# Kernel tuning notes

Measured on AMD Instinct MI355X. Metric: run time of the kernel, lower is better.

Reference implementation:

```python
import jax, jax.numpy as jnp
import numpy as np

B, F, D = 1024, 256, 64  # batch, featureNumb, featureDim


def setup_inputs() -> dict:
    key = jax.random.key(0)
    k1, k2, k3, k4 = jax.random.split(key, 4)
    feature = jax.random.normal(k1, (B, F, D), dtype=jnp.float32)
    indicator = jax.random.normal(k2, (F, D), dtype=jnp.float32)
    # QKVTransformV2(n, D, D): n stacked DxD linear maps of the indicator
    W_qk = jax.random.normal(k3, (2, D, D), dtype=jnp.float32) / np.float32(np.sqrt(D))
    W_qkv = jax.random.normal(k4, (3, D, D), dtype=jnp.float32) / np.float32(np.sqrt(D))
    return {"feature": feature, "indicator": indicator, "W_qk": W_qk, "W_qkv": W_qkv}


def reference(feature, indicator, W_qk, W_qkv):
    d = indicator.shape[-1]
    scale = jnp.asarray(1.0 / np.sqrt(d), feature.dtype)

    # --- gate branch: QKTrans + DotWeight + LTE (straight-through hard threshold) ---
    trans = jnp.einsum('fd,nde->nfe', indicator, W_qk)            # [2,F,D]
    gate_logits = jnp.einsum('id,jd->ij', trans[0], trans[1]) * scale  # [F,F]
    gate = (gate_logits > 0).astype(feature.dtype)                # LTE forward: hard 0/1 gate

    # --- QKV branch, fused form of the rank-1 outer products ---
    # Original: QKV_outer[t,i,j] = qkv[t,i] (x) qkv[t,j]  (DxD rank-1)
    #           input[b,t,i,j,:] = feature[b,i] @ QKV_outer[t,i,j]
    #                            = (feature[b,i] . qkv[t,i]) * qkv[t,j]
    qkv = jnp.einsum('fd,nde->nfe', indicator, W_qkv)             # [3,F,D]
    s = jnp.einsum('bfd,nfd->nbf', feature, qkv)                  # s[t,b,i] = feature[b,i].qkv[t,i]

    # score[b,i,j] = input[b,0,i,j,:] . input[b,1,j,i,:]
    #              = s[0,b,i] * s[1,b,j] * (qkv[1,i] . qkv[0,j])
    cross = jnp.einsum('id,jd->ij', qkv[1], qkv[0])               # [F,F]
    score = s[0][:, :, None] * s[1][:, None, :] * cross[None]     # [B,F,F]
    scoreHat = score * gate[None]                                 # [B,F,F]

    # output[b,i,:] = sum_j scoreHat[b,i,j] * value[b,i,j,:]
    #               = s[2,b,i] * sum_j scoreHat[b,i,j] * qkv[2,j,:]
    out = s[2][:, :, None] * jnp.einsum('bij,jd->bid', scoreHat, qkv[2])  # [B,F,D]
    return out
```

## Files before the change

### kernel.cpp

```cpp
#include <hip/hip_runtime.h>
#include <stdint.h>

#define B 1024
#define F 256
#define D 64

typedef __attribute__((ext_vector_type(8))) short short8;
typedef __attribute__((ext_vector_type(4))) float f32x4;

__device__ __forceinline__ short f2bf(float f) {
    unsigned u = __builtin_bit_cast(unsigned, f);
    u += 0x7fff + ((u >> 16) & 1);
    return (short)(u >> 16);
}
__device__ __forceinline__ float bf2f(short s) {
    unsigned u = ((unsigned)(unsigned short)s) << 16;
    return __builtin_bit_cast(float, u);
}
__device__ __forceinline__ unsigned pk_bf16(float a, float b) {
    unsigned ua = __builtin_bit_cast(unsigned, a) + 0x8000u;
    unsigned ub = __builtin_bit_cast(unsigned, b) + 0x8000u;
    return __builtin_amdgcn_perm(ub, ua, 0x07060302u);
}

__device__ __forceinline__ float dot4(float4 a, float4 b) {
    return a.x * b.x + a.y * b.y + a.z * b.z + a.w * b.w;
}


__global__ void precompute_trans(const float* __restrict__ indicator,
                                 const float* __restrict__ W_qk,
                                 const float* __restrict__ W_qkv,
                                 float* __restrict__ trans,
                                 float* __restrict__ qkv) {
    int idx = blockIdx.x * blockDim.x + threadIdx.x;
    int n   = idx / (F * D);
    int rem = idx - n * (F * D);
    int f   = rem / D;
    int e   = rem - f * D;
    const float* W = (n < 2) ? (W_qk + n * D * D) : (W_qkv + (n - 2) * D * D);
    const float* ind = indicator + f * D;
    float acc = 0.f;
#pragma unroll 8
    for (int d = 0; d < D; ++d) acc += ind[d] * W[d * D + e];
    if (n < 2) trans[n * F * D + f * D + e] = acc;
    else       qkv[(n - 2) * F * D + f * D + e] = acc;
}

__global__ __launch_bounds__(256) void compute_Mt(const float* __restrict__ trans,
                                                  const float* __restrict__ qkv,
                                                  short* __restrict__ At,
                                                  short* __restrict__ q2K) {
    int j = blockIdx.x;
    int i = threadIdx.x;
    const float4* t0 = (const float4*)(trans + i * D);
    const float4* t1 = (const float4*)(trans + F * D + j * D);
    const float4* q1 = (const float4*)(qkv + F * D + i * D);
    const float4* q0 = (const float4*)(qkv + j * D);
    float d0 = 0.f, d1 = 0.f;
#pragma unroll
    for (int k = 0; k < D / 4; ++k) {
        float4 a = t0[k], b = t1[k], c = q1[k], e = q0[k];
        d0 += dot4(a, b);
        d1 += dot4(c, e);
    }
    float v = (d0 > 0.f) ? d1 : 0.f;
    At[((j >> 5) * F + i) * 32 + (j & 31)] = f2bf(v);
    if (j < D) {
        int p = (j & 3) * 16 + (j >> 2);
        q2K[((i >> 5) * D + p) * 32 + (i & 31)] = f2bf(qkv[2 * F * D + i * D + j]);
    }
}

__global__ __launch_bounds__(512, 4) void fused_sg(const float* __restrict__ feature,
                                                   const float* __restrict__ qkv,
                                                   const short* __restrict__ At,
                                                   const short* __restrict__ q2K,
                                                   float* __restrict__ out) {
    int bp  = blockIdx.x;
    int b0  = bp * 2;
    int tid = threadIdx.x;

    __shared__ __align__(16) short q2L[8 * 64 * 32];
    __shared__ __align__(16) short s1L[2 * F];
    __shared__ __align__(16) float gL[2 * F];

    {
        const float4* Qg = (const float4*)q2K;
        float4* Ql = (float4*)q2L;
#pragma unroll
        for (int v = tid; v < 2048; v += 512) Ql[v] = Qg[v];
    }

    {
        int rg = tid >> 4;
        int l  = tid & 15;
#pragma unroll 2
        for (int p = 0; p < 8; ++p) {
            int f = p * 32 + rg;
            float4 fv0 = ((const float4*)(feature + ((size_t)(b0 * F + f)) * D))[l];
            float4 fv1 = ((const float4*)(feature + ((size_t)((b0 + 1) * F + f)) * D))[l];
            float4 q0 = ((const float4*)(qkv + f * D))[l];
            float4 q1 = ((const float4*)(qkv + F * D + f * D))[l];
            float4 q2 = ((const float4*)(qkv + 2 * F * D + f * D))[l];
            float a00 = dot4(fv0, q0);
            float a01 = dot4(fv0, q1);
            float a02 = dot4(fv0, q2);
            float a10 = dot4(fv1, q0);
            float a11 = dot4(fv1, q1);
            float a12 = dot4(fv1, q2);
#pragma unroll
            for (int m = 1; m < 16; m <<= 1) {
                a00 += __shfl_xor(a00, m, 64);
                a01 += __shfl_xor(a01, m, 64);
                a02 += __shfl_xor(a02, m, 64);
                a10 += __shfl_xor(a10, m, 64);
                a11 += __shfl_xor(a11, m, 64);
                a12 += __shfl_xor(a12, m, 64);
            }
            if (l == 0) {
                gL[f]      = a00 * a02;
                gL[F + f]  = a10 * a12;
                s1L[f]     = f2bf(a01);
                s1L[F + f] = f2bf(a11);
            }
        }
    }
    __syncthreads();

    int w    = tid >> 6;
    int lane = tid & 63;
    int l16  = lane & 15;
    int lq   = lane >> 4;
    int kq   = lq * 8;
    int wc   = w & 1;
    int it   = w >> 1;
    int b    = b0 + wc;

    f32x4 acc[4][4];
#pragma unroll
    for (int mt = 0; mt < 4; ++mt)
#pragma unroll
        for (int nt = 0; nt < 4; ++nt) acc[mt][nt] = (f32x4){0.f, 0.f, 0.f, 0.f};

    for (int jt = 0; jt < F / 32; ++jt) {
        short8 sv = *(const short8*)(s1L + wc * F + jt * 32 + kq);
        float sf[8];
#pragma unroll
        for (int e = 0; e < 8; ++e) sf[e] = bf2f(sv[e]);

        short8 bfr[4];
#pragma unroll
        for (int nt = 0; nt < 4; ++nt) {
            int d = nt * 16 + l16;
            short8 qv = *(const short8*)(q2L + (jt * 64 + d) * 32 + kq);
            int4 packed;
            packed.x = pk_bf16(bf2f(qv[0]) * sf[0], bf2f(qv[1]) * sf[1]);
            packed.y = pk_bf16(bf2f(qv[2]) * sf[2], bf2f(qv[3]) * sf[3]);
            packed.z = pk_bf16(bf2f(qv[4]) * sf[4], bf2f(qv[5]) * sf[5]);
            packed.w = pk_bf16(bf2f(qv[6]) * sf[6], bf2f(qv[7]) * sf[7]);
            bfr[nt] = __builtin_bit_cast(short8, packed);
        }
#pragma unroll
        for (int mt = 0; mt < 4; ++mt) {
            short8 af = *(const short8*)(At + ((size_t)jt * F + it * 64 + mt * 16 + l16) * 32 + kq);
#pragma unroll
            for (int nt = 0; nt < 4; ++nt)
                acc[mt][nt] = __builtin_amdgcn_mfma_f32_16x16x32_bf16(
                    af, bfr[nt], acc[mt][nt], 0, 0, 0);
        }
    }

    const float4* g4 = (const float4*)(gL + wc * F + it * 64);
#pragma unroll
    for (int mt = 0; mt < 4; ++mt) {
        float4 gg = g4[mt * 4 + lq];
        float* obase = out + ((size_t)(b * F + it * 64 + mt * 16 + lq * 4)) * D + l16 * 4;
        float4 v0 = {gg.x * acc[mt][0][0], gg.x * acc[mt][1][0],
                     gg.x * acc[mt][2][0], gg.x * acc[mt][3][0]};
        float4 v1 = {gg.y * acc[mt][0][1], gg.y * acc[mt][1][1],
                     gg.y * acc[mt][2][1], gg.y * acc[mt][3][1]};
        float4 v2 = {gg.z * acc[mt][0][2], gg.z * acc[mt][1][2],
                     gg.z * acc[mt][2][2], gg.z * acc[mt][3][2]};
        float4 v3 = {gg.w * acc[mt][0][3], gg.w * acc[mt][1][3],
                     gg.w * acc[mt][2][3], gg.w * acc[mt][3][3]};
        *(float4*)(obase + 0 * D) = v0;
        *(float4*)(obase + 1 * D) = v1;
        *(float4*)(obase + 2 * D) = v2;
        *(float4*)(obase + 3 * D) = v3;
    }
}

extern "C" void kernel_launch(void* const* d_in, const int* in_sizes, int n_in,
                              void* d_out, int out_size, void* d_ws, size_t ws_size,
                              hipStream_t stream) {
    const float* feature   = (const float*)d_in[0];
    const float* indicator = (const float*)d_in[1];
    const float* W_qk      = (const float*)d_in[2];
    const float* W_qkv     = (const float*)d_in[3];
    float* out = (float*)d_out;

    float* ws    = (float*)d_ws;
    float* trans = ws;
    float* qkv   = trans + 2 * F * D;
    short* At    = (short*)(qkv + 3 * F * D);
    short* q2K   = At + F * F;

    hipLaunchKernelGGL(precompute_trans, dim3((5 * F * D) / 256), dim3(256), 0,
                       stream, indicator, W_qk, W_qkv, trans, qkv);
    hipLaunchKernelGGL(compute_Mt, dim3(F), dim3(256), 0, stream, trans, qkv, At, q2K);
    hipLaunchKernelGGL(fused_sg, dim3(B / 2), dim3(512), 0, stream,
                       feature, qkv, At, q2K, out);
}
```

Measured before the change: 144.9 us.

## Double-buffer feature rows into LDS via async global_load_lds in fused_sg

The feature-projection phase now streams each batch pair's feature rows into a double-buffered LDS staging area with direct global-to-LDS loads, in 64-row chunks. This overlaps the next chunk's load with the current chunk's dot products. It adds 32KB of shared memory per block and lowers the launch-bounds occupancy hint from 4 to 2. It also adds a barrier per chunk, so fewer resident blocks could reduce latency hiding in the MFMA phase.

```diff
diff --git a/kernel.cpp b/kernel.cpp
--- a/kernel.cpp
+++ b/kernel.cpp
@@ -25,6 +25,12 @@
 
 __device__ __forceinline__ float dot4(float4 a, float4 b) {
     return a.x * b.x + a.y * b.y + a.z * b.z + a.w * b.w;
+}
+
+__device__ __forceinline__ void gload_lds16(const float* g, float* l) {
+    __builtin_amdgcn_global_load_lds(
+        (const __attribute__((address_space(1))) unsigned int*)g,
+        (__attribute__((address_space(3))) unsigned int*)l, 16, 0, 0);
 }
 
 
@@ -72,7 +78,7 @@
     }
 }
 
-__global__ __launch_bounds__(512, 4) void fused_sg(const float* __restrict__ feature,
+__global__ __launch_bounds__(512, 2) void fused_sg(const float* __restrict__ feature,
                                                    const float* __restrict__ qkv,
                                                    const short* __restrict__ At,
                                                    const short* __restrict__ q2K,
@@ -82,6 +88,7 @@
     int tid = threadIdx.x;
 
     __shared__ __align__(16) short q2L[8 * 64 * 32];
+    __shared__ __align__(16) float fbuf[2][4096];
     __shared__ __align__(16) short s1L[2 * F];
     __shared__ __align__(16) float gL[2 * F];
 
@@ -95,38 +102,50 @@
     {
         int rg = tid >> 4;
         int l  = tid & 15;
-#pragma unroll 2
-        for (int p = 0; p < 8; ++p) {
-            int f = p * 32 + rg;
-            float4 fv0 = ((const float4*)(feature + ((size_t)(b0 * F + f)) * D))[l];
-            float4 fv1 = ((const float4*)(feature + ((size_t)((b0 + 1) * F + f)) * D))[l];
-            float4 q0 = ((const float4*)(qkv + f * D))[l];
-            float4 q1 = ((const float4*)(qkv + F * D + f * D))[l];
-            float4 q2 = ((const float4*)(qkv + 2 * F * D + f * D))[l];
-            float a00 = dot4(fv0, q0);
-            float a01 = dot4(fv0, q1);
-            float a02 = dot4(fv0, q2);
-            float a10 = dot4(fv1, q0);
-            float a11 = dot4(fv1, q1);
-            float a12 = dot4(fv1, q2);
-#pragma unroll
-            for (int m = 1; m < 16; m <<= 1) {
-                a00 += __shfl_xor(a00, m, 64);
-                a01 += __shfl_xor(a01, m, 64);
-                a02 += __shfl_xor(a02, m, 64);
-                a10 += __shfl_xor(a10, m, 64);
-                a11 += __shfl_xor(a11, m, 64);
-                a12 += __shfl_xor(a12, m, 64);
+
+#define STAGE(c, buf)                                                          \
+        {                                                                      \
+            const float* gb = feature +                                        \
+                ((size_t)((b0 + ((c) >> 2)) * F + (((c) & 3) * 64)) * D);      \
+            float* lb = fbuf[buf];                                             \
+            gload_lds16(gb + tid * 4, lb + tid * 4);                           \
+            gload_lds16(gb + 2048 + tid * 4, lb + 2048 + tid * 4);             \
+        }
+
+        STAGE(0, 0)
+        __syncthreads();
+        for (int c = 0; c < 8; ++c) {
+            int buf = c & 1;
+            if (c < 7) STAGE(c + 1, buf ^ 1)
+            int bsel  = c >> 2;
+            int fbase = (c & 3) * 64;
+            const float4* fb = (const float4*)fbuf[buf];
+#pragma unroll
+            for (int q = 0; q < 2; ++q) {
+                int r = q * 32 + rg;
+                int f = fbase + r;
+                float4 fv = fb[r * 16 + l];
+                float4 q0 = ((const float4*)(qkv + f * D))[l];
+                float4 q1 = ((const float4*)(qkv + F * D + f * D))[l];
+                float4 q2 = ((const float4*)(qkv + 2 * F * D + f * D))[l];
+                float a0 = dot4(fv, q0);
+                float a1 = dot4(fv, q1);
+                float a2 = dot4(fv, q2);
+#pragma unroll
+                for (int m = 1; m < 16; m <<= 1) {
+                    a0 += __shfl_xor(a0, m, 64);
+                    a1 += __shfl_xor(a1, m, 64);
+                    a2 += __shfl_xor(a2, m, 64);
+                }
+                if (l == 0) {
+                    gL[bsel * F + f]  = a0 * a2;
+                    s1L[bsel * F + f] = f2bf(a1);
+                }
             }
-            if (l == 0) {
-                gL[f]      = a00 * a02;
-                gL[F + f]  = a10 * a12;
-                s1L[f]     = f2bf(a01);
-                s1L[F + f] = f2bf(a11);
-            }
-        }
-    }
-    __syncthreads();
+            __syncthreads();
+        }
+#undef STAGE
+    }
 
     int w    = tid >> 6;
     int lane = tid & 63;
```

New measurement: 140.9 us (median of 2 runs). 2.8% less time.
